# Optimization experiments

Hardware: AMD Instinct MI355X
Metric: run time of the kernel (lower is better)

## Reference

```python
import jax, jax.numpy as jnp
import numpy as np
import math

B, SQ, SK, D_MODEL, OUT_DIM = 8, 2048, 2048, 1024, 128
MASK_VALUE = -1e6  # torch code fills masked scores with -1000000.0, not -inf


def setup_inputs() -> dict:
    key = jax.random.key(0)
    ks = jax.random.split(key, 10)
    scale = 1.0 / math.sqrt(D_MODEL)
    return {
        "queries": jax.random.normal(ks[0], (B, SQ, D_MODEL), dtype=jnp.float32),
        "keys": jax.random.normal(ks[1], (B, SK, D_MODEL), dtype=jnp.float32),
        "values": jax.random.normal(ks[2], (B, SK, D_MODEL), dtype=jnp.float32),
        "valid_lens": jax.random.randint(ks[3], (B,), 1, SK + 1, dtype=jnp.int32),
        "w_q": jax.random.normal(ks[4], (D_MODEL, OUT_DIM), dtype=jnp.float32) * scale,
        "b_q": jnp.zeros((OUT_DIM,), dtype=jnp.float32),
        "w_k": jax.random.normal(ks[5], (D_MODEL, OUT_DIM), dtype=jnp.float32) * scale,
        "b_k": jnp.zeros((OUT_DIM,), dtype=jnp.float32),
        "w_v": jax.random.normal(ks[6], (D_MODEL, OUT_DIM), dtype=jnp.float32) * scale,
        "b_v": jnp.zeros((OUT_DIM,), dtype=jnp.float32),
    }


def reference(queries, keys, values, valid_lens, w_q, b_q, w_k, b_k, w_v, b_v):
    # QKV projections (LazyLinear equivalents)
    Q = queries @ w_q + b_q   # [B, SQ, OUT_DIM]
    K = keys @ w_k + b_k      # [B, SK, OUT_DIM]
    V = values @ w_v + b_v    # [B, SK, OUT_DIM]
    dim = Q.shape[-1]
    scores = jnp.einsum("bqd,bkd->bqk", Q, K) / jnp.sqrt(jnp.asarray(dim, Q.dtype))
    # masked_softmax: valid_lens [B] -> mask positions >= valid_len on the key axis
    mask = jnp.arange(scores.shape[-1])[None, None, :] < valid_lens[:, None, None]
    scores = jnp.where(mask, scores, jnp.asarray(MASK_VALUE, scores.dtype))
    attn = jax.nn.softmax(scores, axis=-1)
    return jnp.einsum("bqk,bkd->bqd", attn, V)  # [B, SQ, OUT_DIM]
```

## Files before the change

### kernel.cpp

```cpp
#include <hip/hip_runtime.h>
#include <math.h>

constexpr int BATCH  = 8;
constexpr int SEQQ   = 2048;
constexpr int SEQK   = 2048;
constexpr int DMODEL = 1024;
constexpr int ODIM   = 128;

typedef __attribute__((ext_vector_type(8))) short bf16x8;
typedef __attribute__((ext_vector_type(4))) float f32x4;

__device__ inline unsigned short f2bf(float f) {
    union { float f; unsigned int u; } v; v.f = f;
    unsigned int r = v.u + 0x7FFFu + ((v.u >> 16) & 1u);
    return (unsigned short)(r >> 16);
}

__device__ __forceinline__ unsigned int pk2bf(float a, float b) {
    unsigned int ua = __float_as_uint(a) + 0x8000u;
    unsigned int ub = __float_as_uint(b) + 0x8000u;
    return __builtin_amdgcn_perm(ub, ua, 0x07060302u);
}

__device__ __forceinline__ void gl_lds16(const void* g, void* l) {
    __builtin_amdgcn_global_load_lds(
        (const __attribute__((address_space(1))) unsigned int*)g,
        (__attribute__((address_space(3))) unsigned int*)l, 16, 0, 0);
}

__global__ __launch_bounds__(256)
void wtrans_kernel(const float* __restrict__ Wq, const float* __restrict__ Wk,
                   const float* __restrict__ Wv, unsigned short* __restrict__ Wt)
{
    const int which = blockIdx.z;
    const float* __restrict__ W = which == 0 ? Wq : (which == 1 ? Wk : Wv);
    unsigned short* __restrict__ dst = Wt + (size_t)which * DMODEL * ODIM;
    const int k0 = blockIdx.x * 32, n0 = blockIdx.y * 32;
    __shared__ unsigned short T[32][36];
    const int t = threadIdx.x;
    const int r = t >> 3, c = (t & 7) * 4;
    float4 w = *(const float4*)(W + (size_t)(k0 + r) * ODIM + n0 + c);
    T[r][c + 0] = f2bf(w.x); T[r][c + 1] = f2bf(w.y);
    T[r][c + 2] = f2bf(w.z); T[r][c + 3] = f2bf(w.w);
    __syncthreads();
    const int n = t >> 3, k4 = (t & 7) * 4;
    ushort4 o;
    o.x = T[k4 + 0][n]; o.y = T[k4 + 1][n];
    o.z = T[k4 + 2][n]; o.w = T[k4 + 3][n];
    *(ushort4*)(dst + (size_t)(n0 + n) * DMODEL + k0 + k4) = o;
}

__global__ __launch_bounds__(256, 3)
void proj_kernel(const float* __restrict__ Aq, const float* __restrict__ Ak,
                 const float* __restrict__ Av,
                 const unsigned short* __restrict__ Wt_all,
                 const float* __restrict__ bq, const float* __restrict__ bk,
                 const float* __restrict__ bv,
                 unsigned short* __restrict__ Qb, unsigned short* __restrict__ Kb,
                 unsigned short* __restrict__ Vt)
{
    const int which = blockIdx.y;
    const float* __restrict__ A    = which == 0 ? Aq : (which == 1 ? Ak : Av);
    const float* __restrict__ bias = which == 0 ? bq : (which == 1 ? bk : bv);
    const unsigned short* __restrict__ Wt = Wt_all + (size_t)which * DMODEL * ODIM;

    const int row0 = blockIdx.x * 64;
    const int t = threadIdx.x, wave = t >> 6, lane = t & 63;
    const int lrow = lane & 15, quad = lane >> 4;
    const int wrh = (wave & 1) * 32;
    const int wch = (wave >> 1) * 64;

    __shared__ __align__(16) unsigned short As[2][64 * 64];
    __shared__ __align__(16) unsigned short Ws[2][128 * 64];

    f32x4 acc[2][4];
#pragma unroll
    for (int mt = 0; mt < 2; ++mt)
#pragma unroll
        for (int nt = 0; nt < 4; ++nt)
#pragma unroll
            for (int i = 0; i < 4; ++i) acc[mt][nt][i] = 0.f;

    const float* agp[4];
    int awoff[4];
#pragma unroll
    for (int j = 0; j < 4; ++j) {
        const int s = j * 256 + t;
        const int ar = s >> 4, ac = s & 15;
        agp[j]   = A + (size_t)(row0 + ar) * DMODEL + ac * 4;
        awoff[j] = ar * 64 + (((ac >> 1) ^ (ar & 7)) * 8) + (ac & 1) * 4;
    }
    const unsigned short* wgp[4];
    int wloff[4];
#pragma unroll
    for (int j = 0; j < 4; ++j) {
        const int s = j * 256 + t;
        const int wr = s >> 3, wcc = (s & 7) ^ (wr & 7);
        wgp[j]   = Wt + (size_t)wr * DMODEL + wcc * 8;
        wloff[j] = s * 8;
    }

    const int x = lrow & 7;
    float4 areg[4];

#pragma unroll
    for (int j = 0; j < 4; ++j) areg[j] = *(const float4*)(agp[j]);
#pragma unroll
    for (int j = 0; j < 4; ++j) gl_lds16(wgp[j], &Ws[0][wloff[j]]);
#pragma unroll
    for (int j = 0; j < 4; ++j) {
        uint2 p;
        p.x = pk2bf(areg[j].x, areg[j].y);
        p.y = pk2bf(areg[j].z, areg[j].w);
        *(uint2*)&As[0][awoff[j]] = p;
    }
    __syncthreads();

    int cur = 0;
    for (int k0 = 0; k0 < DMODEL; k0 += 64) {
        const bool pf = (k0 + 64) < DMODEL;
        if (pf) {
#pragma unroll
            for (int j = 0; j < 4; ++j)
                areg[j] = *(const float4*)(agp[j] + k0 + 64);
#pragma unroll
            for (int j = 0; j < 4; ++j)
                gl_lds16(wgp[j] + k0 + 64, &Ws[cur ^ 1][wloff[j]]);
        }

#pragma unroll
        for (int ks = 0; ks < 2; ++ks) {
            const int c = (ks * 4 + quad) ^ x;
            bf16x8 af0 = *(const bf16x8*)&As[cur][(wrh + lrow) * 64 + c * 8];
            bf16x8 af1 = *(const bf16x8*)&As[cur][(wrh + 16 + lrow) * 64 + c * 8];
#pragma unroll
            for (int nt = 0; nt < 4; ++nt) {
                const int n = wch + nt * 16 + lrow;
                bf16x8 wf = *(const bf16x8*)&Ws[cur][n * 64 + c * 8];
                acc[0][nt] = __builtin_amdgcn_mfma_f32_16x16x32_bf16(af0, wf, acc[0][nt], 0, 0, 0);
                acc[1][nt] = __builtin_amdgcn_mfma_f32_16x16x32_bf16(af1, wf, acc[1][nt], 0, 0, 0);
            }
        }

        if (pf) {
#pragma unroll
            for (int j = 0; j < 4; ++j) {
                uint2 p;
                p.x = pk2bf(areg[j].x, areg[j].y);
                p.y = pk2bf(areg[j].z, areg[j].w);
                *(uint2*)&As[cur ^ 1][awoff[j]] = p;
            }
        }
        __syncthreads();
        cur ^= 1;
    }

    const float sc = (which == 0) ? 0.08838834764831845f : 1.0f;
    float bv_[4];
#pragma unroll
    for (int nt = 0; nt < 4; ++nt) bv_[nt] = bias[wch + nt * 16 + lrow];

    const int b  = row0 >> 11;
    const int mb = row0 & 2047;

    if (which == 2) {
#pragma unroll
        for (int mt = 0; mt < 2; ++mt)
#pragma unroll
            for (int nt = 0; nt < 4; ++nt) {
                const int n = wch + nt * 16 + lrow;
                ushort4 o;
                o.x = f2bf(acc[mt][nt][0] + bv_[nt]);
                o.y = f2bf(acc[mt][nt][1] + bv_[nt]);
                o.z = f2bf(acc[mt][nt][2] + bv_[nt]);
                o.w = f2bf(acc[mt][nt][3] + bv_[nt]);
                *(ushort4*)(Vt + ((size_t)b * ODIM + n) * SEQK
                            + mb + wrh + mt * 16 + quad * 4) = o;
            }
    } else {
        unsigned short* __restrict__ Ob = (which == 0) ? Qb : Kb;
#pragma unroll
        for (int mt = 0; mt < 2; ++mt)
#pragma unroll
            for (int nt = 0; nt < 4; ++nt)
#pragma unroll
                for (int r = 0; r < 4; ++r) {
                    float val = sc * (acc[mt][nt][r] + bv_[nt]);
                    Ob[(size_t)(row0 + wrh + mt * 16 + quad * 4 + r) * ODIM
                       + wch + nt * 16 + lrow] = f2bf(val);
                }
    }
}

__global__ __launch_bounds__(256, 3)
void flash_kernel(const unsigned short* __restrict__ Qb,
                  const unsigned short* __restrict__ Kb,
                  const unsigned short* __restrict__ Vt,
                  const int* __restrict__ valid_lens,
                  float* __restrict__ Op, float* __restrict__ Lp, int nsplit)
{
    const int b = blockIdx.y, s = blockIdx.z, q0 = blockIdx.x * 64;
    const int skh = SEQK / nsplit;
    const int t = threadIdx.x, wave = t >> 6, lane = t & 63;
    const int lrow = lane & 15, quad = lane >> 4;

    const int valid = valid_lens[b];
    const int vloc  = min(valid - s * skh, skh);

    float* __restrict__ lpart = Lp + (size_t)(s * BATCH + b) * SEQQ + q0;
    float* __restrict__ opart = Op + ((size_t)(s * BATCH + b) * SEQQ + q0) * ODIM;

    if (vloc <= 0) {
        if (t < 64) lpart[t] = 0.f;
        return;
    }

    __shared__ __align__(16) unsigned short Ks[64 * 128];
    __shared__ __align__(16) unsigned short Vs[128 * 64];
    __shared__ __align__(16) unsigned short Ps[4][16][72];

    bf16x8 qf[4];
    {
        const unsigned short* qp =
            Qb + ((size_t)b * SEQQ + q0 + wave * 16 + lrow) * ODIM + quad * 8;
#pragma unroll
        for (int ks = 0; ks < 4; ++ks) qf[ks] = *(const bf16x8*)(qp + ks * 32);
    }

    f32x4 o[8];
#pragma unroll
    for (int nt = 0; nt < 8; ++nt)
#pragma unroll
        for (int i = 0; i < 4; ++i) o[nt][i] = 0.f;
    float lsum[4] = {0.f, 0.f, 0.f, 0.f};

    const unsigned short* kgp[4]; unsigned short* kldst[4];
    const unsigned short* vgp[4]; unsigned short* vldst[4];
    const unsigned short* kbase = Kb + ((size_t)b * SEQK + s * skh) * ODIM;
    const unsigned short* vbase = Vt + (size_t)b * ODIM * SEQK + s * skh;
#pragma unroll
    for (int j = 0; j < 4; ++j) {
        const int sl = j * 256 + t;
        const int kr = sl >> 4, kc = (sl & 15) ^ (kr & 15);
        kgp[j]   = kbase + (size_t)kr * ODIM + kc * 8;
        kldst[j] = &Ks[sl * 8];
        const int vr = sl >> 3, vc = (sl & 7) ^ (vr & 7);
        vgp[j]   = vbase + (size_t)vr * SEQK + vc * 8;
        vldst[j] = &Vs[sl * 8];
    }

    const int x4 = lrow, x3 = lrow & 7;
    const int nch = (vloc + 63) >> 6;

    for (int c = 0; c < nch; ++c) {
        const int k0 = c * 64;
#pragma unroll
        for (int j = 0; j < 4; ++j) {
            gl_lds16(kgp[j] + (size_t)k0 * ODIM, kldst[j]);
            gl_lds16(vgp[j] + k0, vldst[j]);
        }
        __syncthreads();

        f32x4 sv[4];
#pragma unroll
        for (int nt = 0; nt < 4; ++nt)
#pragma unroll
            for (int i = 0; i < 4; ++i) sv[nt][i] = 0.f;
#pragma unroll
        for (int ks = 0; ks < 4; ++ks)
#pragma unroll
            for (int nt = 0; nt < 4; ++nt) {
                const int kr = nt * 16 + lrow;
                const int cc = (ks * 4 + quad) ^ x4;
                bf16x8 kf = *(const bf16x8*)&Ks[(kr * 16 + cc) * 8];
                sv[nt] = __builtin_amdgcn_mfma_f32_16x16x32_bf16(qf[ks], kf, sv[nt], 0, 0, 0);
            }

        if (k0 + 64 > vloc) {
#pragma unroll
            for (int nt = 0; nt < 4; ++nt)
                if (k0 + nt * 16 + lrow >= vloc) {
#pragma unroll
                    for (int i = 0; i < 4; ++i) sv[nt][i] = -1e30f;
                }
        }

#pragma unroll
        for (int nt = 0; nt < 4; ++nt)
#pragma unroll
            for (int r = 0; r < 4; ++r) {
                float p = __expf(sv[nt][r]);
                lsum[r] += p;
                Ps[wave][quad * 4 + r][nt * 16 + lrow] =
                    (unsigned short)((__float_as_uint(p) + 0x8000u) >> 16);
            }

        bf16x8 pf0 = *(const bf16x8*)&Ps[wave][lrow][quad * 8];
        bf16x8 pf1 = *(const bf16x8*)&Ps[wave][lrow][32 + quad * 8];

#pragma unroll
        for (int nt = 0; nt < 8; ++nt) {
            const int vrow = nt * 16 + lrow;
            bf16x8 v0 = *(const bf16x8*)&Vs[(vrow * 8 + (quad ^ x3)) * 8];
            o[nt] = __builtin_amdgcn_mfma_f32_16x16x32_bf16(pf0, v0, o[nt], 0, 0, 0);
        }
#pragma unroll
        for (int nt = 0; nt < 8; ++nt) {
            const int vrow = nt * 16 + lrow;
            bf16x8 v1 = *(const bf16x8*)&Vs[(vrow * 8 + ((4 + quad) ^ x3)) * 8];
            o[nt] = __builtin_amdgcn_mfma_f32_16x16x32_bf16(pf1, v1, o[nt], 0, 0, 0);
        }
        __syncthreads();
    }

#pragma unroll
    for (int msk = 1; msk < 16; msk <<= 1)
#pragma unroll
        for (int r = 0; r < 4; ++r) lsum[r] += __shfl_xor(lsum[r], msk);
    if (lrow == 0) {
#pragma unroll
        for (int r = 0; r < 4; ++r)
            lpart[wave * 16 + quad * 4 + r] = lsum[r];
    }

#pragma unroll
    for (int nt = 0; nt < 8; ++nt)
#pragma unroll
        for (int r = 0; r < 4; ++r)
            opart[(size_t)(wave * 16 + quad * 4 + r) * ODIM + nt * 16 + lrow]
                = o[nt][r];
}

__global__ __launch_bounds__(256)
void combine_kernel(const float* __restrict__ Op, const float* __restrict__ Lp,
                    float* __restrict__ out, int nsplit)
{
    const int idx = blockIdx.x * 256 + threadIdx.x;
    const int row = idx >> 5;
    const size_t SL = (size_t)BATCH * SEQQ;
    float l = 0.f;
    float4 acc = {0.f, 0.f, 0.f, 0.f};
    for (int s = 0; s < nsplit; ++s) {
        float ls = Lp[(size_t)s * SL + row];
        if (ls > 0.f) {
            float4 v = ((const float4*)(Op + (size_t)s * SL * ODIM))[idx];
            acc.x += v.x; acc.y += v.y; acc.z += v.z; acc.w += v.w;
            l += ls;
        }
    }
    const float inv = 1.f / l;
    float4 r;
    r.x = acc.x * inv; r.y = acc.y * inv; r.z = acc.z * inv; r.w = acc.w * inv;
    ((float4*)out)[idx] = r;
}

extern "C" void kernel_launch(void* const* d_in, const int* in_sizes, int n_in,
                              void* d_out, int out_size, void* d_ws, size_t ws_size,
                              hipStream_t stream)
{
    const float* queries    = (const float*)d_in[0];
    const float* keys       = (const float*)d_in[1];
    const float* values     = (const float*)d_in[2];
    const int*   valid_lens = (const int*)d_in[3];
    const float* w_q        = (const float*)d_in[4];
    const float* b_q        = (const float*)d_in[5];
    const float* w_k        = (const float*)d_in[6];
    const float* b_k        = (const float*)d_in[7];
    const float* w_v        = (const float*)d_in[8];
    const float* b_v        = (const float*)d_in[9];
    float* out = (float*)d_out;

    const size_t nQKV = (size_t)BATCH * SEQQ * ODIM;
    unsigned short* Qb = (unsigned short*)d_ws;
    unsigned short* Kb = Qb + nQKV;
    unsigned short* Vt = Kb + nQKV;
    unsigned short* Wt = Vt + nQKV;
    const size_t base = 3 * nQKV * sizeof(unsigned short)
                      + (size_t)3 * DMODEL * ODIM * sizeof(unsigned short);

    int KS = 4;
    if (ws_size < base + 4 * (nQKV * 4 + (size_t)BATCH * SEQQ * 4)) KS = 2;

    float* Op = (float*)((char*)d_ws + base);
    float* Lp = Op + (size_t)KS * nQKV;

    wtrans_kernel<<<dim3(DMODEL / 32, ODIM / 32, 3), 256, 0, stream>>>(w_q, w_k, w_v, Wt);

    proj_kernel<<<dim3((BATCH * SEQQ) / 64, 3), 256, 0, stream>>>(
        queries, keys, values, Wt, b_q, b_k, b_v, Qb, Kb, Vt);

    flash_kernel<<<dim3(SEQQ / 64, BATCH, KS), 256, 0, stream>>>(
        Qb, Kb, Vt, valid_lens, Op, Lp, KS);

    combine_kernel<<<(BATCH * SEQQ * ODIM / 4) / 256, 256, 0, stream>>>(Op, Lp, out, KS);
}
```

Before: 262.4 us.

## Deepen projection GEMM pipeline with two-stage A prefetch and manual waitcnt barriers

Rewrites the projection kernel's K-loop as an unrolled macro step, ping-ponging two register sets so fp32 activation tiles are loaded two iterations ahead instead of one. The `__syncthreads` calls are replaced by explicit `s_waitcnt vmcnt(4) lgkmcnt(0)` plus raw `s_barrier`, fenced by scheduling barriers. The next-step global-to-LDS weight copies can then be waited on while the newer activation loads stay in flight. The aim is to hide more global memory latency in the memory-bound projection. The cost is more registers and fragile hand-written wait counts that depend on in-order vmcnt retirement.

```diff
diff --git a/kernel.cpp b/kernel.cpp
--- a/kernel.cpp
+++ b/kernel.cpp
@@ -50,6 +50,49 @@
     *(ushort4*)(dst + (size_t)(n0 + n) * DMODEL + k0 + k4) = o;
 }
 
+#define PSTEP(T, CUR, REGC, REGN, DO_W, DO_A, DO_WR, WSTR, DO_SYNC)           \
+  {                                                                            \
+    if (DO_W) {                                                                \
+      const int kw = ((T) + 1) * 64;                                           \
+      _Pragma("unroll")                                                        \
+      for (int j = 0; j < 4; ++j)                                              \
+        gl_lds16(wgp[j] + kw, &Ws[(CUR) ^ 1][wloff[j]]);                       \
+    }                                                                          \
+    if (DO_A) {                                                                \
+      const int ka = ((T) + 2) * 64;                                           \
+      _Pragma("unroll")                                                        \
+      for (int j = 0; j < 4; ++j) REGN[j] = *(const float4*)(agp[j] + ka);     \
+    }                                                                          \
+    _Pragma("unroll")                                                          \
+    for (int ks = 0; ks < 2; ++ks) {                                           \
+      const int c = (ks * 4 + quad) ^ x;                                       \
+      bf16x8 af0 = *(const bf16x8*)&As[CUR][(wrh + lrow) * 64 + c * 8];        \
+      bf16x8 af1 = *(const bf16x8*)&As[CUR][(wrh + 16 + lrow) * 64 + c * 8];   \
+      _Pragma("unroll")                                                        \
+      for (int nt = 0; nt < 4; ++nt) {                                         \
+        const int n = wch + nt * 16 + lrow;                                    \
+        bf16x8 wf = *(const bf16x8*)&Ws[CUR][n * 64 + c * 8];                  \
+        acc[0][nt] = __builtin_amdgcn_mfma_f32_16x16x32_bf16(af0, wf, acc[0][nt], 0, 0, 0); \
+        acc[1][nt] = __builtin_amdgcn_mfma_f32_16x16x32_bf16(af1, wf, acc[1][nt], 0, 0, 0); \
+      }                                                                        \
+    }                                                                          \
+    if (DO_WR) {                                                               \
+      _Pragma("unroll")                                                        \
+      for (int j = 0; j < 4; ++j) {                                            \
+        uint2 p;                                                               \
+        p.x = pk2bf(REGC[j].x, REGC[j].y);                                     \
+        p.y = pk2bf(REGC[j].z, REGC[j].w);                                     \
+        *(uint2*)&As[(CUR) ^ 1][awoff[j]] = p;                                 \
+      }                                                                        \
+    }                                                                          \
+    if (DO_SYNC) {                                                             \
+      asm volatile("s_waitcnt " WSTR ::: "memory");                            \
+      __builtin_amdgcn_sched_barrier(0);                                       \
+      __builtin_amdgcn_s_barrier();                                            \
+      __builtin_amdgcn_sched_barrier(0);                                       \
+    }                                                                          \
+  }
+
 __global__ __launch_bounds__(256, 3)
 void proj_kernel(const float* __restrict__ Aq, const float* __restrict__ Ak,
                  const float* __restrict__ Av,
@@ -101,59 +144,32 @@
     }
 
     const int x = lrow & 7;
-    float4 areg[4];
-
-#pragma unroll
-    for (int j = 0; j < 4; ++j) areg[j] = *(const float4*)(agp[j]);
+    float4 ra[4], rb[4];
+
 #pragma unroll
     for (int j = 0; j < 4; ++j) gl_lds16(wgp[j], &Ws[0][wloff[j]]);
+#pragma unroll
+    for (int j = 0; j < 4; ++j) ra[j] = *(const float4*)(agp[j]);
+#pragma unroll
+    for (int j = 0; j < 4; ++j) rb[j] = *(const float4*)(agp[j] + 64);
 #pragma unroll
     for (int j = 0; j < 4; ++j) {
         uint2 p;
-        p.x = pk2bf(areg[j].x, areg[j].y);
-        p.y = pk2bf(areg[j].z, areg[j].w);
+        p.x = pk2bf(ra[j].x, ra[j].y);
+        p.y = pk2bf(ra[j].z, ra[j].w);
         *(uint2*)&As[0][awoff[j]] = p;
     }
-    __syncthreads();
-
-    int cur = 0;
-    for (int k0 = 0; k0 < DMODEL; k0 += 64) {
-        const bool pf = (k0 + 64) < DMODEL;
-        if (pf) {
-#pragma unroll
-            for (int j = 0; j < 4; ++j)
-                areg[j] = *(const float4*)(agp[j] + k0 + 64);
-#pragma unroll
-            for (int j = 0; j < 4; ++j)
-                gl_lds16(wgp[j] + k0 + 64, &Ws[cur ^ 1][wloff[j]]);
-        }
-
-#pragma unroll
-        for (int ks = 0; ks < 2; ++ks) {
-            const int c = (ks * 4 + quad) ^ x;
-            bf16x8 af0 = *(const bf16x8*)&As[cur][(wrh + lrow) * 64 + c * 8];
-            bf16x8 af1 = *(const bf16x8*)&As[cur][(wrh + 16 + lrow) * 64 + c * 8];
-#pragma unroll
-            for (int nt = 0; nt < 4; ++nt) {
-                const int n = wch + nt * 16 + lrow;
-                bf16x8 wf = *(const bf16x8*)&Ws[cur][n * 64 + c * 8];
-                acc[0][nt] = __builtin_amdgcn_mfma_f32_16x16x32_bf16(af0, wf, acc[0][nt], 0, 0, 0);
-                acc[1][nt] = __builtin_amdgcn_mfma_f32_16x16x32_bf16(af1, wf, acc[1][nt], 0, 0, 0);
-            }
-        }
-
-        if (pf) {
-#pragma unroll
-            for (int j = 0; j < 4; ++j) {
-                uint2 p;
-                p.x = pk2bf(areg[j].x, areg[j].y);
-                p.y = pk2bf(areg[j].z, areg[j].w);
-                *(uint2*)&As[cur ^ 1][awoff[j]] = p;
-            }
-        }
-        __syncthreads();
-        cur ^= 1;
-    }
+    asm volatile("s_waitcnt lgkmcnt(0)" ::: "memory");
+    __builtin_amdgcn_sched_barrier(0);
+    __builtin_amdgcn_s_barrier();
+    __builtin_amdgcn_sched_barrier(0);
+
+    for (int kt = 0; kt < 14; kt += 2) {
+        PSTEP(kt,     0, rb, ra, 1, 1, 1, "vmcnt(4) lgkmcnt(0)", 1);
+        PSTEP(kt + 1, 1, ra, rb, 1, 1, 1, "vmcnt(4) lgkmcnt(0)", 1);
+    }
+    PSTEP(14, 0, rb, ra, 1, 0, 1, "vmcnt(0) lgkmcnt(0)", 1);
+    PSTEP(15, 1, ra, rb, 0, 0, 0, "", 0);
 
     const float sc = (which == 0) ? 0.08838834764831845f : 1.0f;
     float bv_[4];
```

Result: faster. 246.7 us (-6.0%).

## Stage full A row-panel in LDS upfront and shrink projection tile to 32 rows

Applied to the files above, without the earlier changes.

The projection kernel now handles 32 rows per block and loads the entire 32x1024 fp32 activation panel up front, converting it to bf16 into a 64KB swizzled LDS buffer. The K loop then streams only weight tiles through a single LDS buffer, separated by explicit waitcnt and barrier pairs. The aim is to issue all activation loads early for more memory parallelism and to double the number of blocks. The cost is single-buffered weight loads that serialize with compute, more total weight traffic because each weight slice is reused over fewer rows, and lower occupancy from the larger LDS footprint.

```diff
diff --git a/kernel.cpp b/kernel.cpp
--- a/kernel.cpp
+++ b/kernel.cpp
@@ -50,7 +50,7 @@
     *(ushort4*)(dst + (size_t)(n0 + n) * DMODEL + k0 + k4) = o;
 }
 
-__global__ __launch_bounds__(256, 3)
+__global__ __launch_bounds__(256, 2)
 void proj_kernel(const float* __restrict__ Aq, const float* __restrict__ Ak,
                  const float* __restrict__ Av,
                  const unsigned short* __restrict__ Wt_all,
@@ -64,34 +64,23 @@
     const float* __restrict__ bias = which == 0 ? bq : (which == 1 ? bk : bv);
     const unsigned short* __restrict__ Wt = Wt_all + (size_t)which * DMODEL * ODIM;
 
-    const int row0 = blockIdx.x * 64;
+    const int row0 = blockIdx.x * 32;
     const int t = threadIdx.x, wave = t >> 6, lane = t & 63;
     const int lrow = lane & 15, quad = lane >> 4;
-    const int wrh = (wave & 1) * 32;
-    const int wch = (wave >> 1) * 64;
-
-    __shared__ __align__(16) unsigned short As[2][64 * 64];
-    __shared__ __align__(16) unsigned short Ws[2][128 * 64];
-
-    f32x4 acc[2][4];
+    const int wch = wave * 32;
+
+    __shared__ __align__(16) unsigned short As[32 * 1024];
+    __shared__ __align__(16) unsigned short Ws[128 * 64];
+
+    f32x4 acc[2][2];
 #pragma unroll
     for (int mt = 0; mt < 2; ++mt)
 #pragma unroll
-        for (int nt = 0; nt < 4; ++nt)
+        for (int nt = 0; nt < 2; ++nt)
 #pragma unroll
             for (int i = 0; i < 4; ++i) acc[mt][nt][i] = 0.f;
 
-    const float* agp[4];
-    int awoff[4];
-#pragma unroll
-    for (int j = 0; j < 4; ++j) {
-        const int s = j * 256 + t;
-        const int ar = s >> 4, ac = s & 15;
-        agp[j]   = A + (size_t)(row0 + ar) * DMODEL + ac * 4;
-        awoff[j] = ar * 64 + (((ac >> 1) ^ (ar & 7)) * 8) + (ac & 1) * 4;
-    }
-    const unsigned short* wgp[4];
-    int wloff[4];
+    const unsigned short* wgp[4]; int wloff[4];
 #pragma unroll
     for (int j = 0; j < 4; ++j) {
         const int s = j * 256 + t;
@@ -100,65 +89,67 @@
         wloff[j] = s * 8;
     }
 
-    const int x = lrow & 7;
-    float4 areg[4];
-
-#pragma unroll
-    for (int j = 0; j < 4; ++j) areg[j] = *(const float4*)(agp[j]);
-#pragma unroll
-    for (int j = 0; j < 4; ++j) gl_lds16(wgp[j], &Ws[0][wloff[j]]);
-#pragma unroll
-    for (int j = 0; j < 4; ++j) {
-        uint2 p;
-        p.x = pk2bf(areg[j].x, areg[j].y);
-        p.y = pk2bf(areg[j].z, areg[j].w);
-        *(uint2*)&As[0][awoff[j]] = p;
+#pragma unroll
+    for (int j = 0; j < 4; ++j) gl_lds16(wgp[j], &Ws[wloff[j]]);
+
+    {
+        const float* abase = A + (size_t)row0 * DMODEL + t * 4;
+        const int cb = t >> 1, h = t & 1;
+#pragma unroll 1
+        for (int bb = 0; bb < 4; ++bb) {
+            float4 v[8];
+#pragma unroll
+            for (int u = 0; u < 8; ++u)
+                v[u] = *(const float4*)(abase + (size_t)(bb * 8 + u) * DMODEL);
+#pragma unroll
+            for (int u = 0; u < 8; ++u) {
+                const int j = bb * 8 + u;
+                uint2 p;
+                p.x = pk2bf(v[u].x, v[u].y);
+                p.y = pk2bf(v[u].z, v[u].w);
+                *(uint2*)&As[j * 1024 + ((cb ^ (j & 7)) << 3) + h * 4] = p;
+            }
+        }
     }
     __syncthreads();
 
-    int cur = 0;
-    for (int k0 = 0; k0 < DMODEL; k0 += 64) {
-        const bool pf = (k0 + 64) < DMODEL;
-        if (pf) {
-#pragma unroll
-            for (int j = 0; j < 4; ++j)
-                areg[j] = *(const float4*)(agp[j] + k0 + 64);
-#pragma unroll
-            for (int j = 0; j < 4; ++j)
-                gl_lds16(wgp[j] + k0 + 64, &Ws[cur ^ 1][wloff[j]]);
-        }
-
+    const int x3 = lrow & 7;
+    const int rA0 = lrow, rA1 = 16 + lrow;
+    const int sw0 = rA0 & 7, sw1 = rA1 & 7;
+
+    for (int s = 0; s < 16; ++s) {
 #pragma unroll
         for (int ks = 0; ks < 2; ++ks) {
-            const int c = (ks * 4 + quad) ^ x;
-            bf16x8 af0 = *(const bf16x8*)&As[cur][(wrh + lrow) * 64 + c * 8];
-            bf16x8 af1 = *(const bf16x8*)&As[cur][(wrh + 16 + lrow) * 64 + c * 8];
-#pragma unroll
-            for (int nt = 0; nt < 4; ++nt) {
+            const int cf = s * 8 + ks * 4 + quad;
+            bf16x8 af0 = *(const bf16x8*)&As[rA0 * 1024 + ((cf ^ sw0) << 3)];
+            bf16x8 af1 = *(const bf16x8*)&As[rA1 * 1024 + ((cf ^ sw1) << 3)];
+#pragma unroll
+            for (int nt = 0; nt < 2; ++nt) {
                 const int n = wch + nt * 16 + lrow;
-                bf16x8 wf = *(const bf16x8*)&Ws[cur][n * 64 + c * 8];
+                bf16x8 wf = *(const bf16x8*)&Ws[(n * 8 + ((ks * 4 + quad) ^ x3)) * 8];
                 acc[0][nt] = __builtin_amdgcn_mfma_f32_16x16x32_bf16(af0, wf, acc[0][nt], 0, 0, 0);
                 acc[1][nt] = __builtin_amdgcn_mfma_f32_16x16x32_bf16(af1, wf, acc[1][nt], 0, 0, 0);
             }
         }
-
-        if (pf) {
-#pragma unroll
-            for (int j = 0; j < 4; ++j) {
-                uint2 p;
-                p.x = pk2bf(areg[j].x, areg[j].y);
-                p.y = pk2bf(areg[j].z, areg[j].w);
-                *(uint2*)&As[cur ^ 1][awoff[j]] = p;
-            }
-        }
-        __syncthreads();
-        cur ^= 1;
+        if (s < 15) {
+            asm volatile("s_waitcnt lgkmcnt(0)" ::: "memory");
+            __builtin_amdgcn_sched_barrier(0);
+            __builtin_amdgcn_s_barrier();
+            __builtin_amdgcn_sched_barrier(0);
+#pragma unroll
+            for (int j = 0; j < 4; ++j)
+                gl_lds16(wgp[j] + (s + 1) * 64, &Ws[wloff[j]]);
+            asm volatile("s_waitcnt vmcnt(0)" ::: "memory");
+            __builtin_amdgcn_sched_barrier(0);
+            __builtin_amdgcn_s_barrier();
+            __builtin_amdgcn_sched_barrier(0);
+        }
     }
 
     const float sc = (which == 0) ? 0.08838834764831845f : 1.0f;
-    float bv_[4];
-#pragma unroll
-    for (int nt = 0; nt < 4; ++nt) bv_[nt] = bias[wch + nt * 16 + lrow];
+    float bv_[2];
+#pragma unroll
+    for (int nt = 0; nt < 2; ++nt) bv_[nt] = bias[wch + nt * 16 + lrow];
 
     const int b  = row0 >> 11;
     const int mb = row0 & 2047;
@@ -167,7 +158,7 @@
 #pragma unroll
         for (int mt = 0; mt < 2; ++mt)
 #pragma unroll
-            for (int nt = 0; nt < 4; ++nt) {
+            for (int nt = 0; nt < 2; ++nt) {
                 const int n = wch + nt * 16 + lrow;
                 ushort4 o;
                 o.x = f2bf(acc[mt][nt][0] + bv_[nt]);
@@ -175,18 +166,18 @@
                 o.z = f2bf(acc[mt][nt][2] + bv_[nt]);
                 o.w = f2bf(acc[mt][nt][3] + bv_[nt]);
                 *(ushort4*)(Vt + ((size_t)b * ODIM + n) * SEQK
-                            + mb + wrh + mt * 16 + quad * 4) = o;
+                            + mb + mt * 16 + quad * 4) = o;
             }
     } else {
         unsigned short* __restrict__ Ob = (which == 0) ? Qb : Kb;
 #pragma unroll
         for (int mt = 0; mt < 2; ++mt)
 #pragma unroll
-            for (int nt = 0; nt < 4; ++nt)
+            for (int nt = 0; nt < 2; ++nt)
 #pragma unroll
                 for (int r = 0; r < 4; ++r) {
                     float val = sc * (acc[mt][nt][r] + bv_[nt]);
-                    Ob[(size_t)(row0 + wrh + mt * 16 + quad * 4 + r) * ODIM
+                    Ob[(size_t)(row0 + mt * 16 + quad * 4 + r) * ODIM
                        + wch + nt * 16 + lrow] = f2bf(val);
                 }
     }
@@ -386,7 +377,7 @@
 
     wtrans_kernel<<<dim3(DMODEL / 32, ODIM / 32, 3), 256, 0, stream>>>(w_q, w_k, w_v, Wt);
 
-    proj_kernel<<<dim3((BATCH * SEQQ) / 64, 3), 256, 0, stream>>>(
+    proj_kernel<<<dim3((BATCH * SEQQ) / 32, 3), 256, 0, stream>>>(
         queries, keys, values, Wt, b_q, b_k, b_v, Qb, Kb, Vt);
 
     flash_kernel<<<dim3(SEQQ / 64, BATCH, KS), 256, 0, stream>>>(
```

Measured after the change: 268.1 us. +2.2%, slower.
